# Performance work log

Hardware: AMD Instinct MI355X
Metric: run time of the kernel (lower is better)

The kernel has to match this reference:

```python
import jax, jax.numpy as jnp
import numpy as np

N = 50000    # total nodes in batched graph
E = 800000   # total edges
G = 512      # number of graphs in batch
R = 19       # num_rels (edge types)
D = 64       # hidden dim (dims = [64,64,64])
EMB = D + 1  # embedding dim after concatenating nucleotide scalar
HID = 128
FP = 166     # fingerprint bits


def setup_inputs() -> dict:
    key = jax.random.key(0)
    ks = jax.random.split(key, 24)
    s = 0.05
    inp = {
        "src": jax.random.randint(ks[0], (E,), 0, N, dtype=jnp.int32),
        "dst": jax.random.randint(ks[1], (E,), 0, N, dtype=jnp.int32),
        "etypes": jax.random.randint(ks[2], (E,), 0, R, dtype=jnp.int32),
        "node2graph": jnp.sort(jax.random.randint(ks[3], (N,), 0, G, dtype=jnp.int32)),
        "nuc": jax.random.uniform(ks[4], (N,), dtype=jnp.float32),
        # RelGraphConv layer 0: in_dim=1 (in-degree feature)
        "W0": jax.random.normal(ks[5], (R, 1, D), jnp.float32) * s,
        "b0": jnp.zeros((D,), jnp.float32),
        "L0": jax.random.normal(ks[6], (1, D), jnp.float32) * s,
        # RelGraphConv layer 1
        "W1": jax.random.normal(ks[7], (R, D, D), jnp.float32) * s,
        "b1": jnp.zeros((D,), jnp.float32),
        "L1": jax.random.normal(ks[8], (D, D), jnp.float32) * s,
        # RelGraphConv layer 2 (output layer, no activation)
        "W2": jax.random.normal(ks[9], (R, D, D), jnp.float32) * s,
        "b2": jnp.zeros((D,), jnp.float32),
        "L2": jax.random.normal(ks[10], (D, D), jnp.float32) * s,
        # GlobalAttentionPooling gate: Linear(EMB, 1)
        "gate_w": jax.random.normal(ks[11], (EMB, 1), jnp.float32) * s,
        "gate_b": jnp.zeros((1,), jnp.float32),
        # Attributor MLP: Linear(65,128)+ReLU, Linear(128,166)+Sigmoid
        "A1": jax.random.normal(ks[12], (EMB, HID), jnp.float32) * s,
        "ab1": jnp.zeros((HID,), jnp.float32),
        "A2": jax.random.normal(ks[13], (HID, FP), jnp.float32) * s,
        "ab2": jnp.zeros((FP,), jnp.float32),
    }
    return inp


def reference(src, dst, etypes, node2graph, nuc,
              W0, b0, L0, W1, b1, L1, W2, b2, L2,
              gate_w, gate_b, A1, ab1, A2, ab2):
    # input feature: in-degree per node, shape [N, 1]
    deg = jax.ops.segment_sum(jnp.ones((E,), jnp.float32), dst, num_segments=N)[:, None]

    def relconv(h, W, L, b, act):
        # per-relation projection of all nodes: [N, R, dout]
        proj = jnp.einsum('nd,rdo->nro', h, W)
        msg = proj[src, etypes]                               # [E, dout] gather
        agg = jax.ops.segment_sum(msg, dst, num_segments=N)   # scatter-sum to dst nodes
        out = agg + h @ L + b                                 # self-loop + bias (DGL defaults)
        return jax.nn.relu(out) if act else out

    h = relconv(deg, W0, L0, b0, True)
    h = relconv(h,   W1, L1, b1, True)
    h = relconv(h,   W2, L2, b2, False)

    # nucs=True: concat nucleotide scalar -> [N, 65]
    emb = jnp.concatenate([h, nuc[:, None]], axis=1)

    # GlobalAttentionPooling: per-graph segment softmax over gate scores
    gate = (emb @ gate_w + gate_b)[:, 0]                       # [N]
    gmax = jax.ops.segment_max(gate, node2graph, num_segments=G)
    ex = jnp.exp(gate - gmax[node2graph])
    denom = jax.ops.segment_sum(ex, node2graph, num_segments=G)
    alpha = ex / denom[node2graph]
    fp = jax.ops.segment_sum(alpha[:, None] * emb, node2graph, num_segments=G)  # [G, 65]

    # Attributor (dropout is identity in eval)
    h1 = jax.nn.relu(fp @ A1 + ab1)
    out = jax.nn.sigmoid(h1 @ A2 + ab2)                        # [G, 166]
    return out, emb
```

## Files before the change

### kernel.cpp

```cpp
#include <hip/hip_runtime.h>
#include <cstdint>

static constexpr int NN = 50000;
static constexpr int NE = 800000;
static constexpr int NG = 512;
static constexpr int NR = 19;
static constexpr int DD = 64;
static constexpr int EMB = 65;
static constexpr int HID = 128;
static constexpr int FP = 166;
static constexpr int NEP = NE + NR * 16;
static constexpr int NMSG = NE + 304;
static constexpr int SCB5 = (NN + 511) / 512;
static constexpr int EB5  = (NE + 511) / 512;
static constexpr int ET5  = (NE + 4095) / 4096;
static constexpr int WPB512 = (2 * NR * 8 * 64 + 511) / 512;

typedef __fp16 h2 __attribute__((ext_vector_type(2)));
typedef _Float16 F16x2 __attribute__((ext_vector_type(2)));
typedef _Float16 hf8 __attribute__((ext_vector_type(8)));
typedef float f32x4 __attribute__((ext_vector_type(4)));
typedef unsigned u32x4 __attribute__((ext_vector_type(4)));
typedef int i32x4 __attribute__((ext_vector_type(4)));

union U4H8 { u32x4 u; hf8 h; };

__device__ __forceinline__ hf8 as_hf8(u32x4 u) { U4H8 c; c.u = u; return c.h; }

__device__ __forceinline__ float dot2f(unsigned a, unsigned b, float c) {
    union { unsigned u; h2 h; } ua, ub;
    ua.u = a; ub.u = b;
    return __builtin_amdgcn_fdot2(ua.h, ub.h, c, false);
}

__device__ __forceinline__ unsigned pack2(float a, float b) {
    union { h2 h; unsigned u; } r;
    r.h = __builtin_amdgcn_cvt_pkrtz(a, b);
    return r.u;
}

__device__ __forceinline__ void pkAtomicAdd(unsigned* addr, float lo, float hi) {
    unsigned u = pack2(lo, hi);
#if __has_builtin(__builtin_amdgcn_global_atomic_fadd_v2f16)
    union { unsigned u; F16x2 h; } c; c.u = u;
    __builtin_amdgcn_global_atomic_fadd_v2f16((F16x2*)addr, c.h);
#else
    asm volatile("global_atomic_pk_add_f16 %0, %1, off" :: "v"(addr), "v"(u) : "memory");
#endif
}

__device__ __forceinline__ float half_at(unsigned v, int idx) {
    union { unsigned u; h2 h; } c; c.u = v;
    return (float)c.h[idx];
}

__device__ __forceinline__ int lbound(const int* __restrict__ a, int key) {
    int lo = 0, hi = NN;
    while (lo < hi) {
        int mid = (lo + hi) >> 1;
        if (a[mid] < key) lo = mid + 1; else hi = mid;
    }
    return lo;
}

__global__ __launch_bounds__(512) void kd1(const int* __restrict__ dst, const int* __restrict__ et,
                                           int* __restrict__ degi, int* __restrict__ cnt19) {
    const int b = blockIdx.x;
    const int t = threadIdx.x;
    if (b < ET5) {
        __shared__ int lcnt[8][NR];
        const int lane = t & 63;
        const int wid = t >> 6;
        const int wbase = (b * 8 + wid) * 512;
        int cnt = 0;
#pragma unroll
        for (int i = 0; i < 8; ++i) {
            int e = wbase + i * 64 + lane;
            int myet = (e < NE) ? et[e] : -1;
#pragma unroll
            for (int r = 0; r < NR; ++r) {
                unsigned long long bm = __ballot(myet == r);
                if (lane == r) cnt += (int)__popcll(bm);
            }
        }
        if (lane < NR) lcnt[wid][lane] = cnt;
        __syncthreads();
        if (t < NR) {
            int s = 0;
#pragma unroll
            for (int wv = 0; wv < 8; ++wv) s += lcnt[wv][t];
            if (s) atomicAdd(&cnt19[t], s);
        }
    } else {
        int e = (b - ET5) * 512 + t;
        if (e < NE) atomicAdd(&degi[dst[e]], 1);
    }
}

__global__ __launch_bounds__(512) void kd2(const int* __restrict__ degi, int* __restrict__ part,
                                           const int* __restrict__ cnt19, int* __restrict__ pbase,
                                           int* __restrict__ cur19, int* __restrict__ batchptr,
                                           unsigned* __restrict__ hpk0, unsigned* __restrict__ hpk1,
                                           unsigned* __restrict__ sdp, unsigned char* __restrict__ ets,
                                           const float* __restrict__ W1, const float* __restrict__ W2,
                                           unsigned* __restrict__ wpk1, unsigned* __restrict__ wpk2) {
    const int b = blockIdx.x;
    const int t = threadIdx.x;
    if (b < SCB5) {
        __shared__ int red[512];
        int idx = b * 512 + t;
        red[t] = (idx < NN) ? degi[idx] : 0;
        __syncthreads();
#pragma unroll
        for (int s = 256; s > 0; s >>= 1) {
            if (t < s) red[t] += red[t + s];
            __syncthreads();
        }
        if (t == 0) part[b] = red[0];
    } else if (b == SCB5) {
        __shared__ int spb[NR + 1];
        if (t == 0) {
            int run = 0;
            for (int r = 0; r < NR; ++r) {
                spb[r] = run; pbase[r] = run; cur19[r] = run; batchptr[r] = run >> 4;
                run += (cnt19[r] + 15) & ~15;
            }
            spb[NR] = run; pbase[NR] = run; batchptr[NR] = run >> 4;
        }
        if (t < 32) hpk0[(size_t)NN * 32 + t] = 0;
        else if (t < 64) hpk1[(size_t)NN * 32 + (t - 32)] = 0;
        __syncthreads();
        int r = t >> 4, i = t & 15;
        if (r < NR) {
            int cnt = cnt19[r];
            int tail = spb[r + 1] - spb[r] - cnt;
            if (i < tail) {
                int pos = spb[r] + cnt + i;
                sdp[pos] = (unsigned)NN | ((unsigned)NN << 16);
                ets[pos] = 0;
            }
        }
    } else {
        int tt = (b - SCB5 - 1) * 512 + t;
        if (tt >= 2 * NR * 8 * 64) return;
        int which = tt >= NR * 8 * 64;
        int t2 = tt - which * NR * 8 * 64;
        const float* W = which ? W2 : W1;
        unsigned* wpk = which ? wpk2 : wpk1;
        int lane = t2 & 63;
        int f = (t2 >> 6) & 7;
        int r = t2 >> 9;
        int kh = f >> 2, ct = f & 3;
        int kbase = kh * 32 + (lane >> 4) * 8;
        int col = (ct >> 1) * 32 + 2 * (lane & 15) + (ct & 1);
        const float* wr = W + (size_t)r * DD * DD;
        u32x4 out;
#pragma unroll
        for (int p = 0; p < 4; ++p)
            out[p] = pack2(wr[(kbase + 2 * p) * DD + col], wr[(kbase + 2 * p + 1) * DD + col]);
        *((u32x4*)wpk + t2) = out;
    }
}

__global__ __launch_bounds__(512) void kd3(const int* __restrict__ degi, const int* __restrict__ part,
                                           int* __restrict__ dstoff, int* __restrict__ cur,
                                           const int* __restrict__ src, const int* __restrict__ dst,
                                           const int* __restrict__ et, int* __restrict__ cur19,
                                           unsigned* __restrict__ sdp, unsigned char* __restrict__ ets) {
    const int b = blockIdx.x;
    const int t = threadIdx.x;
    if (b < SCB5) {
        __shared__ int sp[512];
        __shared__ int s[512];
        sp[t] = (t < SCB5) ? part[t] : 0;
        int idx = b * 512 + t;
        int v = (idx < NN) ? degi[idx] : 0;
        s[t] = v;
        __syncthreads();
#pragma unroll
        for (int d = 1; d < 512; d <<= 1) {
            int x1 = (t >= d) ? sp[t - d] : 0;
            int x2 = (t >= d) ? s[t - d] : 0;
            __syncthreads();
            sp[t] += x1;
            s[t] += x2;
            __syncthreads();
        }
        int boff = (b == 0) ? 0 : sp[b - 1];
        int excl = boff + ((t == 0) ? 0 : s[t - 1]);
        if (idx < NN) { dstoff[idx] = excl; cur[idx] = excl; }
        if (idx == NN - 1) { dstoff[NN] = NE; cur[NN] = NE; }
    } else {
        __shared__ int wcnt[8][NR];
        __shared__ int lb[NR];
        __shared__ int woff[8][NR];
        const int bb = b - SCB5;
        const int lane = t & 63;
        const int wid = t >> 6;
        int e = bb * 512 + t;
        int myet = -1, d = 0, sv = 0;
        if (e < NE) { myet = et[e]; d = dst[e]; sv = src[e]; }
        const unsigned long long below = (lane == 63) ? ~0ull >> 1 : ((1ull << lane) - 1);
        int myrank = 0, cnt_r = 0;
#pragma unroll
        for (int r = 0; r < NR; ++r) {
            unsigned long long m = __ballot(myet == r);
            if (myet == r) myrank = (int)__popcll(m & below);
            if (lane == r) cnt_r = (int)__popcll(m);
        }
        if (lane < NR) wcnt[wid][lane] = cnt_r;
        __syncthreads();
        if (t < NR) {
            int run = 0, c[8];
#pragma unroll
            for (int wv = 0; wv < 8; ++wv) { c[wv] = wcnt[wv][t]; }
#pragma unroll
            for (int wv = 0; wv < 8; ++wv) { woff[wv][t] = run; run += c[wv]; }
            lb[t] = run ? atomicAdd(&cur19[t], run) : 0;
        }
        __syncthreads();
        if (e < NE) {
            int pos = lb[myet] + woff[wid][myet] + myrank;
            sdp[pos] = (unsigned)sv | ((unsigned)d << 16);
            ets[pos] = (unsigned char)myet;
        }
    }
}

__global__ __launch_bounds__(256) void kperm(const unsigned* __restrict__ sdp, const unsigned char* __restrict__ ets,
                                             const int* __restrict__ pbase, const int* __restrict__ degi,
                                             int* __restrict__ cur, int* __restrict__ perm,
                                             unsigned* __restrict__ msg0) {
    int p = blockIdx.x * 256 + threadIdx.x;
    if (p >= pbase[NR]) return;
    unsigned sd = sdp[p];
    int s = (int)(sd & 0xffffu);
    int d = (int)(sd >> 16);
    int deg = (s < NN) ? degi[s] : 0;
    unsigned etv = ets[p];
    int slot = atomicAdd(&cur[d], 1);
    perm[p] = slot;
    msg0[slot] = (etv << 16) | (unsigned)deg;
}

__global__ __launch_bounds__(256) void kf0m(const unsigned* __restrict__ msg0, const int* __restrict__ dstoff,
                                            const float* __restrict__ W0, const float* __restrict__ L0,
                                            const float* __restrict__ b0, unsigned* __restrict__ hpk0) {
    __shared__ float Lw[NR * DD];
    for (int i = threadIdx.x; i < NR * DD; i += 256) Lw[i] = W0[i];
    __syncthreads();
    int lane = threadIdx.x & 63;
    int wid = __builtin_amdgcn_readfirstlane(threadIdx.x >> 6);
    int n = blockIdx.x * 4 + wid;
    if (n >= NN) return;
    int r0 = dstoff[n], r1 = dstoff[n + 1];
    float deg = (float)(r1 - r0);
    float acc = b0[lane] + deg * L0[lane];
    for (int row = r0; row < r1; ++row) {
        unsigned v = msg0[row];
        acc += (float)(v & 0xffffu) * Lw[(v >> 16) * DD + lane];
    }
    acc = fmaxf(acc, 0.f);
    float other = __shfl_xor(acc, 1);
    if ((lane & 1) == 0) hpk0[n * 32 + (lane >> 1)] = pack2(acc, other);
}

__global__ __launch_bounds__(256) void ktpass(const int* __restrict__ src, const int* __restrict__ dst,
                                              const int* __restrict__ et, const int* __restrict__ degi,
                                              float* __restrict__ T) {
    int e = blockIdx.x * 256 + threadIdx.x;
    if (e < NE) unsafeAtomicAdd(&T[dst[e] * NR + et[e]], (float)degi[src[e]]);
}

__global__ __launch_bounds__(256) void kf0(const float* __restrict__ T, const float* __restrict__ W0,
                                           const float* __restrict__ L0, const float* __restrict__ b0,
                                           const int* __restrict__ degi, unsigned* __restrict__ hpk0) {
    int lane = threadIdx.x & 63;
    int wid = __builtin_amdgcn_readfirstlane(threadIdx.x >> 6);
    int n = blockIdx.x * 4 + wid;
    if (n >= NN) return;
    float w0r[NR];
#pragma unroll
    for (int r = 0; r < NR; ++r) w0r[r] = W0[r * DD + lane];
    float acc = b0[lane] + (float)degi[n] * L0[lane];
    const float* Trow = T + n * NR;
#pragma unroll
    for (int r = 0; r < NR; ++r) acc += Trow[r] * w0r[r];
    acc = fmaxf(acc, 0.f);
    float other = __shfl_xor(acc, 1);
    if ((lane & 1) == 0) hpk0[n * 32 + (lane >> 1)] = pack2(acc, other);
}

template <bool STORE>
__global__ __launch_bounds__(256) void kmsgm(const unsigned* __restrict__ sdp, const int* __restrict__ perm,
                                             const int* __restrict__ batchptr, const unsigned* __restrict__ hpk,
                                             const unsigned* __restrict__ wpk, unsigned* __restrict__ out) {
    const int lane = threadIdx.x & 63;
    int wid = __builtin_amdgcn_readfirstlane(threadIdx.x >> 6);
    int gw = blockIdx.x * 4 + wid;
    const int nwaves = gridDim.x * 4;
    const int totB = batchptr[NR];
    int chunk = (totB + nwaves - 1) / nwaves;
    int b0 = gw * chunk;
    int b1 = min(b0 + chunk, totB);
    if (b0 >= b1) return;

    int r = 0;
    while (batchptr[r + 1] <= b0) ++r;

    hf8 Bf[8];
    auto loadB = [&](int rr) {
        const u32x4* wq = (const u32x4*)wpk;
#pragma unroll
        for (int f = 0; f < 8; ++f) Bf[f] = as_hf8(wq[(rr * 8 + f) * 64 + lane]);
    };
    loadB(r);
    int rend = batchptr[r + 1];

    const int qk = lane >> 4;
    const int lm = lane & 15;

    for (int b = b0; b < b1; ++b) {
        while (b >= rend) {
            ++r;
            rend = batchptr[r + 1];
            if (b < rend) loadB(r);
        }
        int base = b << 4;
        int s = (int)(sdp[base + lm] & 0xffffu);
        const unsigned* hr = hpk + (size_t)s * 32;
        hf8 a0 = as_hf8(*(const u32x4*)(hr + (qk << 2)));
        hf8 a1 = as_hf8(*(const u32x4*)(hr + 16 + (qk << 2)));
        i32x4 d4;
        if constexpr (STORE) {
            d4 = *(const i32x4*)(perm + base + (qk << 2));
        } else {
            u32x4 sd4 = *(const u32x4*)(sdp + base + (qk << 2));
#pragma unroll
            for (int j = 0; j < 4; ++j) d4[j] = (int)(sd4[j] >> 16);
        }

        f32x4 acc0 = {0.f, 0.f, 0.f, 0.f};
        f32x4 acc1 = {0.f, 0.f, 0.f, 0.f};
        f32x4 acc2 = {0.f, 0.f, 0.f, 0.f};
        f32x4 acc3 = {0.f, 0.f, 0.f, 0.f};
        acc0 = __builtin_amdgcn_mfma_f32_16x16x32_f16(a0, Bf[0], acc0, 0, 0, 0);
        acc1 = __builtin_amdgcn_mfma_f32_16x16x32_f16(a0, Bf[1], acc1, 0, 0, 0);
        acc2 = __builtin_amdgcn_mfma_f32_16x16x32_f16(a0, Bf[2], acc2, 0, 0, 0);
        acc3 = __builtin_amdgcn_mfma_f32_16x16x32_f16(a0, Bf[3], acc3, 0, 0, 0);
        acc0 = __builtin_amdgcn_mfma_f32_16x16x32_f16(a1, Bf[4], acc0, 0, 0, 0);
        acc1 = __builtin_amdgcn_mfma_f32_16x16x32_f16(a1, Bf[5], acc1, 0, 0, 0);
        acc2 = __builtin_amdgcn_mfma_f32_16x16x32_f16(a1, Bf[6], acc2, 0, 0, 0);
        acc3 = __builtin_amdgcn_mfma_f32_16x16x32_f16(a1, Bf[7], acc3, 0, 0, 0);

#pragma unroll
        for (int j = 0; j < 4; ++j) {
            if constexpr (STORE) {
                unsigned pk0 = pack2(acc0[j], acc1[j]);
                unsigned pk1 = pack2(acc2[j], acc3[j]);
                unsigned long long v = ((unsigned long long)pk1 << 32) | pk0;
                *(unsigned long long*)(out + (size_t)d4[j] * 32 + 2 * lm) = v;
            } else {
                unsigned* ag = out + (size_t)d4[j] * 32 + lm;
                pkAtomicAdd(ag, acc0[j], acc1[j]);
                pkAtomicAdd(ag + 16, acc2[j], acc3[j]);
            }
        }
    }
}

template <bool ACT, bool WRITE_EMB, bool MSGMODE>
__global__ __launch_bounds__(256) void kfin(const unsigned* __restrict__ agm, const int* __restrict__ dstoff,
                                            const unsigned* __restrict__ hpk_in, const float* __restrict__ L,
                                            const float* __restrict__ bvec, unsigned* __restrict__ hpk_out,
                                            float* __restrict__ embp, const float* __restrict__ nuc,
                                            const float* __restrict__ gatew, const float* __restrict__ gateb,
                                            float* __restrict__ gate) {
    __shared__ unsigned Lp[32 * 64];
    for (int i = threadIdx.x; i < 2048; i += 256) {
        int kp = i >> 6, o = i & 63;
        Lp[i] = pack2(L[(2 * kp) * DD + o], L[(2 * kp + 1) * DD + o]);
    }
    __syncthreads();
    int lane = threadIdx.x & 63;
    int wid = __builtin_amdgcn_readfirstlane(threadIdx.x >> 6);
    int n = blockIdx.x * 4 + wid;
    if (n >= NN) return;
    float acc = bvec[lane];
    if constexpr (MSGMODE) {
        const int dwp = lane & 15;
        const int ro = lane >> 4;
        int r0 = dstoff[n], r1 = dstoff[n + 1];
        float m0a = 0.f, m1a = 0.f, m2a = 0.f, m3a = 0.f;
        for (int row = r0; row < r1; row += 4) {
            int rr = row + ro;
            unsigned long long v = 0;
            if (rr < r1) v = *(const unsigned long long*)(agm + (size_t)rr * 32 + 2 * dwp);
            unsigned vlo = (unsigned)v, vhi = (unsigned)(v >> 32);
            m0a += half_at(vlo, 0); m1a += half_at(vlo, 1);
            m2a += half_at(vhi, 0); m3a += half_at(vhi, 1);
        }
        m0a += __shfl_xor(m0a, 16); m0a += __shfl_xor(m0a, 32);
        m1a += __shfl_xor(m1a, 16); m1a += __shfl_xor(m1a, 32);
        m2a += __shfl_xor(m2a, 16); m2a += __shfl_xor(m2a, 32);
        m3a += __shfl_xor(m3a, 16); m3a += __shfl_xor(m3a, 32);
        int dp = (lane & 31) >> 1;
        float s0 = __shfl(m0a, dp), s1 = __shfl(m1a, dp);
        float s2 = __shfl(m2a, dp), s3 = __shfl(m3a, dp);
        float sel_lo = (lane & 1) ? s1 : s0;
        float sel_hi = (lane & 1) ? s3 : s2;
        acc += (lane >= 32) ? sel_hi : sel_lo;
    } else {
        acc += half_at(agm[(size_t)n * 32 + (lane >> 1)], lane & 1);
    }
    const unsigned* hr = hpk_in + n * 32;
    float a0 = 0.f, a1 = 0.f, a2 = 0.f, a3 = 0.f;
#pragma unroll
    for (int k4 = 0; k4 < 8; ++k4) {
        a0 = dot2f(hr[4 * k4 + 0], Lp[(4 * k4 + 0) * 64 + lane], a0);
        a1 = dot2f(hr[4 * k4 + 1], Lp[(4 * k4 + 1) * 64 + lane], a1);
        a2 = dot2f(hr[4 * k4 + 2], Lp[(4 * k4 + 2) * 64 + lane], a2);
        a3 = dot2f(hr[4 * k4 + 3], Lp[(4 * k4 + 3) * 64 + lane], a3);
    }
    acc += (a0 + a1) + (a2 + a3);
    if (ACT) acc = fmaxf(acc, 0.f);
    if constexpr (WRITE_EMB) {
        embp[(size_t)n * EMB + lane] = acc;
        float nv = nuc[n];
        if (lane == 0) embp[(size_t)n * EMB + 64] = nv;
        float v = acc * gatew[lane];
#pragma unroll
        for (int s = 32; s >= 1; s >>= 1) v += __shfl_xor(v, s);
        if (lane == 0) gate[n] = v + nv * gatew[64] + gateb[0];
    } else {
        float other = __shfl_xor(acc, 1);
        if ((lane & 1) == 0) hpk_out[n * 32 + (lane >> 1)] = pack2(acc, other);
    }
}

__global__ __launch_bounds__(128) void kpoolmlp(const int* __restrict__ n2g, const float* __restrict__ gate,
                                                const float* __restrict__ emb, const float* __restrict__ A1,
                                                const float* __restrict__ ab1, const float* __restrict__ A2,
                                                const float* __restrict__ ab2, float* __restrict__ out) {
    __shared__ float red[128];
    __shared__ float c64[2];
    __shared__ float fv[EMB];
    __shared__ float h1[HID];
    int g = blockIdx.x;
    int t = threadIdx.x;
    int lo = lbound(n2g, g);
    int hi = lbound(n2g, g + 1);

    float m = -INFINITY;
    for (int i = lo + t; i < hi; i += 128) m = fmaxf(m, gate[i]);
    red[t] = m;
    __syncthreads();
    for (int s = 64; s > 0; s >>= 1) {
        if (t < s) red[t] = fmaxf(red[t], red[t + s]);
        __syncthreads();
    }
    m = red[0];
    __syncthreads();

    float sum = 0.f;
    for (int i = lo + t; i < hi; i += 128) sum += __expf(gate[i] - m);
    red[t] = sum;
    __syncthreads();
    for (int s = 64; s > 0; s >>= 1) {
        if (t < s) red[t] += red[t + s];
        __syncthreads();
    }
    float denom = red[0];
    __syncthreads();

    const int lane = t & 63;
    const int wv = t >> 6;
    float acc = 0.f, acc64 = 0.f;
    for (int i = lo + wv; i < hi; i += 2) {
        float wt = __expf(gate[i] - m);
        acc += wt * emb[(size_t)i * EMB + lane];
        if (lane == 0) acc64 += wt * emb[(size_t)i * EMB + 64];
    }
    red[t] = acc;
    if (lane == 0) c64[wv] = acc64;
    __syncthreads();
    if (t < 64) {
        float s = red[t] + red[64 + t];
        fv[t] = (hi > lo) ? s / denom : 0.f;
    } else if (t == 64) {
        float s = c64[0] + c64[1];
        fv[64] = (hi > lo) ? s / denom : 0.f;
    }
    __syncthreads();

    float a = ab1[t];
    for (int d = 0; d < EMB; ++d) a += fv[d] * A1[d * HID + t];
    h1[t] = fmaxf(a, 0.f);
    __syncthreads();
    for (int o = t; o < FP; o += HID) {
        float v = ab2[o];
        for (int k = 0; k < HID; ++k) v += h1[k] * A2[k * FP + o];
        out[(size_t)g * FP + o] = 1.f / (1.f + __expf(-v));
    }
}

extern "C" void kernel_launch(void* const* d_in, const int* in_sizes, int n_in,
                              void* d_out, int out_size, void* d_ws, size_t ws_size,
                              hipStream_t stream) {
    const int* src = (const int*)d_in[0];
    const int* dst = (const int*)d_in[1];
    const int* et = (const int*)d_in[2];
    const int* n2g = (const int*)d_in[3];
    const float* nuc = (const float*)d_in[4];
    const float* W0 = (const float*)d_in[5];
    const float* b0 = (const float*)d_in[6];
    const float* L0 = (const float*)d_in[7];
    const float* W1 = (const float*)d_in[8];
    const float* b1 = (const float*)d_in[9];
    const float* L1 = (const float*)d_in[10];
    const float* W2 = (const float*)d_in[11];
    const float* b2 = (const float*)d_in[12];
    const float* L2 = (const float*)d_in[13];
    const float* gatew = (const float*)d_in[14];
    const float* gateb = (const float*)d_in[15];
    const float* A1 = (const float*)d_in[16];
    const float* ab1 = (const float*)d_in[17];
    const float* A2 = (const float*)d_in[18];
    const float* ab2 = (const float*)d_in[19];
    (void)in_sizes; (void)n_in; (void)out_size;

    float* out0 = (float*)d_out;
    float* embp = (float*)d_out + (size_t)NG * FP;

    char* w = (char*)d_ws;
    size_t off = 0;
    auto alloc = [&](size_t bytes) { size_t r = off; off = (off + bytes + 255) & ~(size_t)255; return r; };

    size_t o_degi = alloc(NN * 4);
    size_t o_cnt  = alloc(NR * 4);
    size_t zero_small = off;
    size_t o_T    = alloc((size_t)NN * NR * 4);
    size_t zero_big = off;
    size_t o_hpk0 = alloc((size_t)(NN + 1) * 32 * 4);
    size_t o_hpk1 = alloc((size_t)(NN + 1) * 32 * 4);
    size_t o_pb   = alloc((NR + 1) * 4);
    size_t o_cur19= alloc(NR * 4);
    size_t o_bp   = alloc((NR + 1) * 4);
    size_t o_sdp  = alloc((size_t)NEP * 4);
    size_t o_ets  = alloc((size_t)NEP);
    size_t o_perm = alloc((size_t)NEP * 4);
    size_t o_msg0 = alloc((size_t)NMSG * 4);
    size_t o_doff = alloc((size_t)(NN + 1) * 4);
    size_t o_cur  = alloc((size_t)(NN + 1) * 4);
    size_t o_part = alloc((size_t)SCB5 * 4);
    size_t o_wpk1 = alloc((size_t)NR * 8 * 64 * 16);
    size_t o_wpk2 = alloc((size_t)NR * 8 * 64 * 16);
    size_t o_gate = alloc(NN * 4);
    size_t o_msg  = off;
    size_t need_store = o_msg + (size_t)NMSG * 128;
    bool use_store = ws_size >= need_store;

    int* degi = (int*)(w + o_degi);
    int* cnt19 = (int*)(w + o_cnt);
    float* T = (float*)(w + o_T);
    unsigned* hpk0 = (unsigned*)(w + o_hpk0);
    unsigned* hpk1 = (unsigned*)(w + o_hpk1);
    int* pbase = (int*)(w + o_pb);
    int* cur19 = (int*)(w + o_cur19);
    int* batchptr = (int*)(w + o_bp);
    unsigned* sdp = (unsigned*)(w + o_sdp);
    unsigned char* ets = (unsigned char*)(w + o_ets);
    int* perm = (int*)(w + o_perm);
    unsigned* msg0 = (unsigned*)(w + o_msg0);
    int* dstoff = (int*)(w + o_doff);
    int* cur = (int*)(w + o_cur);
    int* part = (int*)(w + o_part);
    unsigned* wpk1 = (unsigned*)(w + o_wpk1);
    unsigned* wpk2 = (unsigned*)(w + o_wpk2);
    float* gate = (float*)(w + o_gate);
    unsigned* msg = (unsigned*)(w + o_msg);

    const int EB  = (NE + 255) / 256;
    const int EBP = (NEP + 255) / 256;
    const int NW  = (NN + 3) / 4;

    hipMemsetAsync(w, 0, use_store ? zero_small : zero_big, stream);

    kd1<<<ET5 + EB5, 512, 0, stream>>>(dst, et, degi, cnt19);
    kd2<<<SCB5 + 1 + WPB512, 512, 0, stream>>>(degi, part, cnt19, pbase, cur19, batchptr,
                                               hpk0, hpk1, sdp, ets, W1, W2, wpk1, wpk2);
    kd3<<<SCB5 + EB5, 512, 0, stream>>>(degi, part, dstoff, cur, src, dst, et, cur19, sdp, ets);

    if (use_store) {
        kperm<<<EBP, 256, 0, stream>>>(sdp, ets, pbase, degi, cur, perm, msg0);
        kf0m<<<NW, 256, 0, stream>>>(msg0, dstoff, W0, L0, b0, hpk0);

        kmsgm<true><<<1024, 256, 0, stream>>>(sdp, perm, batchptr, hpk0, wpk1, msg);
        kfin<true, false, true><<<NW, 256, 0, stream>>>(msg, dstoff, hpk0, L1, b1, hpk1,
                                                        nullptr, nullptr, nullptr, nullptr, nullptr);
        kmsgm<true><<<1024, 256, 0, stream>>>(sdp, perm, batchptr, hpk1, wpk2, msg);
        kfin<false, true, true><<<NW, 256, 0, stream>>>(msg, dstoff, hpk1, L2, b2, nullptr,
                                                        embp, nuc, gatew, gateb, gate);
    } else {
        ktpass<<<EB, 256, 0, stream>>>(src, dst, et, degi, T);
        kf0<<<NW, 256, 0, stream>>>(T, W0, L0, b0, degi, hpk0);
        hipMemsetAsync(msg, 0, (size_t)NN * 32 * 4, stream);
        kmsgm<false><<<1024, 256, 0, stream>>>(sdp, nullptr, batchptr, hpk0, wpk1, msg);
        kfin<true, false, false><<<NW, 256, 0, stream>>>(msg, nullptr, hpk0, L1, b1, hpk1,
                                                         nullptr, nullptr, nullptr, nullptr, nullptr);
        hipMemsetAsync(msg, 0, (size_t)NN * 32 * 4, stream);
        kmsgm<false><<<1024, 256, 0, stream>>>(sdp, nullptr, batchptr, hpk1, wpk2, msg);
        kfin<false, true, false><<<NW, 256, 0, stream>>>(msg, nullptr, hpk1, L2, b2, nullptr,
                                                         embp, nuc, gatew, gateb, gate);
    }

    kpoolmlp<<<NG, 128, 0, stream>>>(n2g, gate, embp, A1, ab1, A2, ab2, out0);
}
```

Measured before the change: 299.7 us.

## Replace layer-0 per-edge message list with per-node relation histogram via packed atomics

```diff
diff --git a/kernel.cpp b/kernel.cpp
--- a/kernel.cpp
+++ b/kernel.cpp
@@ -15,6 +15,7 @@
 static constexpr int EB5  = (NE + 511) / 512;
 static constexpr int ET5  = (NE + 4095) / 4096;
 static constexpr int WPB512 = (2 * NR * 8 * 64 + 511) / 512;
+static constexpr int THW = 10;
 
 typedef __fp16 h2 __attribute__((ext_vector_type(2)));
 typedef _Float16 F16x2 __attribute__((ext_vector_type(2)));
@@ -103,7 +104,9 @@
                                            unsigned* __restrict__ hpk0, unsigned* __restrict__ hpk1,
                                            unsigned* __restrict__ sdp, unsigned char* __restrict__ ets,
                                            const float* __restrict__ W1, const float* __restrict__ W2,
-                                           unsigned* __restrict__ wpk1, unsigned* __restrict__ wpk2) {
+                                           unsigned* __restrict__ wpk1, unsigned* __restrict__ wpk2,
+                                           const int* __restrict__ src, const int* __restrict__ dst,
+                                           const int* __restrict__ et, unsigned* __restrict__ Th) {
     const int b = blockIdx.x;
     const int t = threadIdx.x;
     if (b < SCB5) {
@@ -140,7 +143,7 @@
                 ets[pos] = 0;
             }
         }
-    } else {
+    } else if (b < SCB5 + 1 + WPB512) {
         int tt = (b - SCB5 - 1) * 512 + t;
         if (tt >= 2 * NR * 8 * 64) return;
         int which = tt >= NR * 8 * 64;
@@ -159,6 +162,15 @@
         for (int p = 0; p < 4; ++p)
             out[p] = pack2(wr[(kbase + 2 * p) * DD + col], wr[(kbase + 2 * p + 1) * DD + col]);
         *((u32x4*)wpk + t2) = out;
+    } else {
+        int e = (b - (SCB5 + 1 + WPB512)) * 512 + t;
+        if (e < NE) {
+            float fd = (float)degi[src[e]];
+            int d = dst[e], r = et[e];
+            unsigned* addr = Th + (size_t)d * THW + (r >> 1);
+            if (r & 1) pkAtomicAdd(addr, 0.f, fd);
+            else pkAtomicAdd(addr, fd, 0.f);
+        }
     }
 }
 
@@ -227,42 +239,40 @@
     }
 }
 
-__global__ __launch_bounds__(256) void kperm(const unsigned* __restrict__ sdp, const unsigned char* __restrict__ ets,
-                                             const int* __restrict__ pbase, const int* __restrict__ degi,
-                                             int* __restrict__ cur, int* __restrict__ perm,
-                                             unsigned* __restrict__ msg0) {
+__global__ __launch_bounds__(256) void kperm(const unsigned* __restrict__ sdp, const int* __restrict__ pbase,
+                                             int* __restrict__ cur, int* __restrict__ perm) {
     int p = blockIdx.x * 256 + threadIdx.x;
     if (p >= pbase[NR]) return;
-    unsigned sd = sdp[p];
-    int s = (int)(sd & 0xffffu);
-    int d = (int)(sd >> 16);
-    int deg = (s < NN) ? degi[s] : 0;
-    unsigned etv = ets[p];
-    int slot = atomicAdd(&cur[d], 1);
-    perm[p] = slot;
-    msg0[slot] = (etv << 16) | (unsigned)deg;
-}
-
-__global__ __launch_bounds__(256) void kf0m(const unsigned* __restrict__ msg0, const int* __restrict__ dstoff,
+    perm[p] = atomicAdd(&cur[sdp[p] >> 16], 1);
+}
+
+__global__ __launch_bounds__(256) void kf0t(const unsigned* __restrict__ Th, const int* __restrict__ dstoff,
                                             const float* __restrict__ W0, const float* __restrict__ L0,
                                             const float* __restrict__ b0, unsigned* __restrict__ hpk0) {
-    __shared__ float Lw[NR * DD];
-    for (int i = threadIdx.x; i < NR * DD; i += 256) Lw[i] = W0[i];
-    __syncthreads();
     int lane = threadIdx.x & 63;
     int wid = __builtin_amdgcn_readfirstlane(threadIdx.x >> 6);
     int n = blockIdx.x * 4 + wid;
     if (n >= NN) return;
+    float w0r[20];
+#pragma unroll
+    for (int r = 0; r < NR; ++r) w0r[r] = W0[r * DD + lane];
+    w0r[19] = 0.f;
     int r0 = dstoff[n], r1 = dstoff[n + 1];
-    float deg = (float)(r1 - r0);
-    float acc = b0[lane] + deg * L0[lane];
-    for (int row = r0; row < r1; ++row) {
-        unsigned v = msg0[row];
-        acc += (float)(v & 0xffffu) * Lw[(v >> 16) * DD + lane];
+    float acc = b0[lane] + (float)(r1 - r0) * L0[lane];
+    const unsigned* tr = Th + (size_t)n * THW;
+#pragma unroll
+    for (int p = 0; p < THW; ++p) {
+        unsigned v = tr[p];
+        acc += half_at(v, 0) * w0r[2 * p] + half_at(v, 1) * w0r[2 * p + 1];
     }
     acc = fmaxf(acc, 0.f);
     float other = __shfl_xor(acc, 1);
     if ((lane & 1) == 0) hpk0[n * 32 + (lane >> 1)] = pack2(acc, other);
+}
+
+__global__ __launch_bounds__(256) void khist_fb(const int* __restrict__ dst, int* __restrict__ degi) {
+    int e = blockIdx.x * 256 + threadIdx.x;
+    if (e < NE) atomicAdd(&degi[dst[e]], 1);
 }
 
 __global__ __launch_bounds__(256) void ktpass(const int* __restrict__ src, const int* __restrict__ dst,
@@ -538,6 +548,7 @@
 
     size_t o_degi = alloc(NN * 4);
     size_t o_cnt  = alloc(NR * 4);
+    size_t o_Th   = alloc((size_t)NN * THW * 4);
     size_t zero_small = off;
     size_t o_T    = alloc((size_t)NN * NR * 4);
     size_t zero_big = off;
@@ -549,7 +560,6 @@
     size_t o_sdp  = alloc((size_t)NEP * 4);
     size_t o_ets  = alloc((size_t)NEP);
     size_t o_perm = alloc((size_t)NEP * 4);
-    size_t o_msg0 = alloc((size_t)NMSG * 4);
     size_t o_doff = alloc((size_t)(NN + 1) * 4);
     size_t o_cur  = alloc((size_t)(NN + 1) * 4);
     size_t o_part = alloc((size_t)SCB5 * 4);
@@ -562,6 +572,7 @@
 
     int* degi = (int*)(w + o_degi);
     int* cnt19 = (int*)(w + o_cnt);
+    unsigned* Th = (unsigned*)(w + o_Th);
     float* T = (float*)(w + o_T);
     unsigned* hpk0 = (unsigned*)(w + o_hpk0);
     unsigned* hpk1 = (unsigned*)(w + o_hpk1);
@@ -571,7 +582,6 @@
     unsigned* sdp = (unsigned*)(w + o_sdp);
     unsigned char* ets = (unsigned char*)(w + o_ets);
     int* perm = (int*)(w + o_perm);
-    unsigned* msg0 = (unsigned*)(w + o_msg0);
     int* dstoff = (int*)(w + o_doff);
     int* cur = (int*)(w + o_cur);
     int* part = (int*)(w + o_part);
@@ -587,13 +597,14 @@
     hipMemsetAsync(w, 0, use_store ? zero_small : zero_big, stream);
 
     kd1<<<ET5 + EB5, 512, 0, stream>>>(dst, et, degi, cnt19);
-    kd2<<<SCB5 + 1 + WPB512, 512, 0, stream>>>(degi, part, cnt19, pbase, cur19, batchptr,
-                                               hpk0, hpk1, sdp, ets, W1, W2, wpk1, wpk2);
+    kd2<<<SCB5 + 1 + WPB512 + EB5, 512, 0, stream>>>(degi, part, cnt19, pbase, cur19, batchptr,
+                                                     hpk0, hpk1, sdp, ets, W1, W2, wpk1, wpk2,
+                                                     src, dst, et, Th);
     kd3<<<SCB5 + EB5, 512, 0, stream>>>(degi, part, dstoff, cur, src, dst, et, cur19, sdp, ets);
 
     if (use_store) {
-        kperm<<<EBP, 256, 0, stream>>>(sdp, ets, pbase, degi, cur, perm, msg0);
-        kf0m<<<NW, 256, 0, stream>>>(msg0, dstoff, W0, L0, b0, hpk0);
+        kperm<<<EBP, 256, 0, stream>>>(sdp, pbase, cur, perm);
+        kf0t<<<NW, 256, 0, stream>>>(Th, dstoff, W0, L0, b0, hpk0);
 
         kmsgm<true><<<1024, 256, 0, stream>>>(sdp, perm, batchptr, hpk0, wpk1, msg);
         kfin<true, false, true><<<NW, 256, 0, stream>>>(msg, dstoff, hpk0, L1, b1, hpk1,
```

After: 326.8 us. 1.09x slower.
